# Optimization experiments

Hardware: AMD Instinct MI355X
Metric: run time of the kernel (lower is better)

## Reference

```python
import jax, jax.numpy as jnp
import numpy as np

B, N, D, R, E = 512, 32, 300, 5, 256
V_SENSE, V_GLOBAL = 20000, 50000  # last_idx_senses, last_idx_globals - last_idx_senses


def setup_inputs() -> dict:
    key = jax.random.key(0)
    ks = jax.random.split(key, 10)
    x = jax.random.normal(ks[0], (B, N, D), jnp.float32)
    edge_index = jax.random.randint(ks[1], (B, 2, E), 0, N)
    edge_type = jnp.sort(jax.random.randint(ks[2], (B, E), 0, R), axis=-1)
    # parameters (xavier-ish scales)
    conv_W = jax.random.normal(ks[3], (R, D, D), jnp.float32) * np.float32(1.0 / np.sqrt(D))
    W0 = jax.random.normal(ks[4], (D, D), jnp.float32) * np.float32(np.sqrt(2.0 / (D + D)))
    update_gate = jnp.ones((1,), jnp.float32)
    glob_W = jax.random.normal(ks[5], (V_GLOBAL, D), jnp.float32) * np.float32(1.0 / np.sqrt(D))
    glob_b = jnp.zeros((V_GLOBAL,), jnp.float32)
    sense_W = jax.random.normal(ks[6], (V_SENSE, D), jnp.float32) * np.float32(1.0 / np.sqrt(D))
    sense_b = jnp.zeros((V_SENSE,), jnp.float32)
    memory0 = jnp.zeros((N, D), jnp.float32)  # initial persisted memory (zeros vector broadcast)
    return dict(x=x, edge_index=edge_index, edge_type=edge_type, conv_W=conv_W, W0=W0,
                update_gate=update_gate, glob_W=glob_W, glob_b=glob_b,
                sense_W=sense_W, sense_b=sense_b, memory0=memory0)


def reference(x, edge_index, edge_type, conv_W, W0, update_gate, glob_W, glob_b, sense_W, sense_b, memory0):
    R_ = conv_W.shape[0]
    N_ = x.shape[1]

    def step(mem, inp):
        xs, ei, et = inp                      # [N,D], [2,E], [E]
        src, dst = ei[0], ei[1]
        # per-relation transformed features (GCNConv, bias=False)
        xw = jnp.einsum('nd,rde->rne', xs, conv_W)          # [R,N,D]
        # per-relation degrees with self-loops (PyG GCNConv symmetric norm)
        onehot = jax.nn.one_hot(et, R_, dtype=xs.dtype)     # [E,R]
        deg = 1.0 + jax.ops.segment_sum(onehot, dst, num_segments=N_)  # [N,R]
        dinv = jax.lax.rsqrt(deg)                           # [N,R]
        coeff = dinv[src, et] * dinv[dst, et]               # [E]
        msg = coeff[:, None] * xw[et, src]                  # [E,D]
        agg = jax.ops.segment_sum(msg, dst, num_segments=N_)  # sum over relations' convs
        self_term = jnp.einsum('rnd,nr->nd', xw, dinv * dinv)  # self-loop of each GCNConv
        composite = agg + self_term
        # prevlayer_connection = eye(N) @ (x @ W_0) = x @ W_0
        proposed = composite + xs @ W0
        new_mem = update_gate * proposed + (1.0 - update_gate) * mem  # rgcn_conv, persisted
        x1 = jax.nn.relu(new_mem)[0]                        # current node features [D]
        return new_mem, x1

    _, x1_all = jax.lax.scan(step, memory0, (x, edge_index, edge_type))  # [B,D]
    logits_g = x1_all @ glob_W.T + glob_b                   # [B,V_GLOBAL]
    logits_s = x1_all @ sense_W.T + sense_b                 # [B,V_SENSE]
    return (jax.nn.log_softmax(logits_g, axis=-1), jax.nn.log_softmax(logits_s, axis=-1))
```

## Files before the change

kernel.cpp:

```cpp
#include <hip/hip_runtime.h>
#include <stdint.h>

#define BDIM   512
#define NNODE  32
#define DDIM   300
#define NREL   5
#define NEDGE  256
#define VGLOB  50000
#define VSENSE 20000

#define K1PAD  1856
#define K2PAD  320
#define TG_GLOB  391
#define TG_SENSE 157
#define TGTOT  548
#define GROWS  50048
#define SROWS  20096
#define WROWS  70144
#define NCHUNK 3
#define KCH    10
#define NSCH   16
#define SCHL   32

typedef __attribute__((ext_vector_type(8))) short short8;
typedef __attribute__((ext_vector_type(4))) float f32x4;

__device__ __forceinline__ unsigned short f2bf(float x) {
    unsigned int u = __float_as_uint(x);
    u += 0x7fffu + ((u >> 16) & 1u);
    return (unsigned short)(u >> 16);
}

__device__ __forceinline__ float powi(float x, int n) {
    float r = 1.f, p = x;
    while (n) { if (n & 1) r *= p; p *= p; n >>= 1; }
    return r;
}

#define AS1 __attribute__((address_space(1)))
#define AS3 __attribute__((address_space(3)))
__device__ __forceinline__ void gload16(const void* gp, void* lp) {
    __builtin_amdgcn_global_load_lds((AS1 void*)gp, (AS3 void*)lp, 16, 0, 0);
}

__global__ __launch_bounds__(256) void k_prep_z(
    const float* __restrict__ x, const int* __restrict__ ei,
    const int* __restrict__ et, unsigned short* __restrict__ Zb)
{
    int b = blockIdx.x, t = threadIdx.x;
    __shared__ int   cnt[NNODE * NREL];
    __shared__ float dinv[NNODE * NREL];
    __shared__ int   ssrc[NEDGE];
    __shared__ int   sdst[NEDGE];
    __shared__ int   setp[NEDGE];
    __shared__ float z[6][DDIM];

    const int* src = ei + (size_t)b * 2 * NEDGE;
    const int* dst = src + NEDGE;
    const int* etb = et + (size_t)b * NEDGE;

    if (t < NNODE * NREL) cnt[t] = 0;
    __syncthreads();
    if (t < NEDGE) {
        int s = src[t], d = dst[t], r = etb[t];
        ssrc[t] = s; sdst[t] = d; setp[t] = r;
        atomicAdd(&cnt[d * NREL + r], 1);
    }
    __syncthreads();
    if (t < NNODE * NREL) dinv[t] = rsqrtf(1.0f + (float)cnt[t]);
    __syncthreads();

    const float* xb = x + (size_t)b * NNODE * DDIM;
    for (int d = t; d < DDIM; d += 256) {
        float x0 = xb[d];
#pragma unroll
        for (int r = 0; r < NREL; r++) { float c = dinv[r]; z[r][d] = c * c * x0; }
        z[5][d] = x0;
    }
    __syncthreads();
    for (int e = 0; e < NEDGE; e++) {
        if (sdst[e] != 0) continue;
        int s = ssrc[e], r = setp[e];
        float coeff = dinv[s * NREL + r] * dinv[r];
        const float* xs = xb + (size_t)s * DDIM;
        for (int d = t; d < DDIM; d += 256) z[r][d] += coeff * xs[d];
    }
    __syncthreads();
    unsigned short* zo = Zb + (size_t)b * K1PAD;
    for (int k = t; k < K1PAD; k += 256) {
        unsigned short v = 0;
        if (k < 6 * DDIM) { int r = k / DDIM, d = k - r * DDIM; v = f2bf(z[r][d]); }
        zo[k] = v;
    }
}

__global__ __launch_bounds__(256) void k_prep_w(
    const float* __restrict__ convW, const float* __restrict__ W0f,
    unsigned short* __restrict__ Wcb)
{
    int idx = blockIdx.x * 256 + threadIdx.x;
    if (idx >= 384 * K1PAD) return;
    int n = idx / K1PAD, k = idx - n * K1PAD;
    float v = 0.f;
    if (n < DDIM && k < 6 * DDIM) {
        int r = k / DDIM, d = k - r * DDIM;
        v = (r < NREL) ? convW[((size_t)r * DDIM + d) * DDIM + n]
                       : W0f[(size_t)d * DDIM + n];
    }
    Wcb[idx] = f2bf(v);
}

__global__ __launch_bounds__(256) void k_conv_w2(
    const float* __restrict__ globW, const float* __restrict__ senseW,
    unsigned short* __restrict__ Wgb)
{
    int idx = blockIdx.x * 256 + threadIdx.x;
    int row = idx / 80, kq = (idx - row * 80) * 4;
    unsigned int p0 = 0, p1 = 0;
    if (kq < DDIM) {
        const float* srcp = nullptr;
        if (row < GROWS) { if (row < VGLOB) srcp = globW + (size_t)row * DDIM; }
        else { int sr = row - GROWS; if (sr < VSENSE) srcp = senseW + (size_t)sr * DDIM; }
        if (srcp) {
            float4 v = *(const float4*)(srcp + kq);
            p0 = (unsigned int)f2bf(v.x) | ((unsigned int)f2bf(v.y) << 16);
            p1 = (unsigned int)f2bf(v.z) | ((unsigned int)f2bf(v.w) << 16);
        }
    }
    uint2 pp; pp.x = p0; pp.y = p1;
    *(uint2*)(Wgb + (size_t)row * K2PAD + kq) = pp;
}

template<int MODE>
__global__ __launch_bounds__(256) void k_gemm_b(
    const unsigned short* __restrict__ A, int ldk, int nk, int kchunk,
    int tiles0,
    const unsigned short* __restrict__ B0, int ldb0,
    const float* __restrict__ bias0, float* __restrict__ C0, long ldc0,
    int nstore0, const float* __restrict__ lse0, int tilebase0,
    const unsigned short* __restrict__ B1, int ldb1,
    const float* __restrict__ bias1, float* __restrict__ C1, long ldc1,
    int nstore1, const float* __restrict__ lse1, int tilebase1,
    float* __restrict__ pmax, float* __restrict__ psum)
{
    __shared__ __align__(16) char Alds[128 * 128];
    __shared__ __align__(16) char Blds[128 * 128];

    int t = threadIdx.x;
    int tile, mrep;
    if constexpr (MODE == 0) {
        tile = blockIdx.x; mrep = blockIdx.y;
    } else {
        int i = blockIdx.x + TGTOT * blockIdx.y;
        if (i < 2176) { int g = i >> 5, r = i & 31; tile = g * 8 + (r & 7); mrep = r >> 3; }
        else          { int j = i - 2176; tile = 544 + (j & 3); mrep = j >> 2; }
    }

    const unsigned short* Bp; const float *bias, *lse; float* Cout;
    long ldc; int ldb, nstore, tileidx, tloc;
    if (tile < tiles0) {
        Bp = B0; bias = bias0; Cout = C0; lse = lse0; ldc = ldc0;
        ldb = ldb0; nstore = nstore0; tloc = tile; tileidx = tilebase0 + tile;
    } else {
        tloc = tile - tiles0;
        Bp = B1; bias = bias1; Cout = C1; lse = lse1; ldc = ldc1;
        ldb = ldb1; nstore = nstore1; tileidx = tilebase1 + tloc;
    }
    int n0 = tloc * 128;
    int m0 = mrep * 128;

    int kt_lo = 0, kt_hi = nk >> 6;
    if constexpr (MODE == 0) {
        if (kchunk > 0) {
            kt_lo = blockIdx.z * kchunk;
            int hi = kt_lo + kchunk;
            if (hi < kt_hi) kt_hi = hi;
            Cout += (size_t)blockIdx.z * (BDIM * 304);
        }
    }

    int lane = t & 63, wid = t >> 6;
    int wm = wid >> 1, wn = wid & 1;
    int l15 = lane & 15, lq = lane >> 4;

    int trow = t >> 3;
    int sb = ((t & 7) << 4) ^ ((trow & 7) << 4);
    const char* Ag = (const char*)A + (size_t)(m0 + trow) * (ldk * 2) + sb;
    const char* Bg = (const char*)Bp + (size_t)(n0 + trow) * (ldb * 2) + sb;
    char* Al = Alds + t * 16;
    char* Bl = Blds + t * 16;
    size_t a32 = (size_t)32 * (ldk * 2);
    size_t b32 = (size_t)32 * (ldb * 2);

    int sw = (l15 & 7) << 4;
    int aoff0 = (lq * 16) ^ sw;
    int aoff1 = (64 + lq * 16) ^ sw;
    const char* Arow = Alds + (wm * 64 + l15) * 128;
    const char* Brow = Blds + (wn * 64 + l15) * 128;

    f32x4 acc[4][4] = {};

    for (int kt = kt_lo; kt < kt_hi; ++kt) {
        int k0b = kt << 7;
        const char* Agk = Ag + k0b;
        const char* Bgk = Bg + k0b;
#pragma unroll
        for (int c = 0; c < 4; c++) {
            gload16(Agk + c * a32, Al + c * 4096);
            gload16(Bgk + c * b32, Bl + c * 4096);
        }
        __syncthreads();
        short8 afr[4][2], bfr[4][2];
#pragma unroll
        for (int i = 0; i < 4; i++) {
            const char* Ab = Arow + i * (16 * 128);
            const char* Bb = Brow + i * (16 * 128);
            afr[i][0] = *(const short8*)(Ab + aoff0);
            afr[i][1] = *(const short8*)(Ab + aoff1);
            bfr[i][0] = *(const short8*)(Bb + aoff0);
            bfr[i][1] = *(const short8*)(Bb + aoff1);
        }
#pragma unroll
        for (int ks = 0; ks < 2; ks++)
#pragma unroll
            for (int mi = 0; mi < 4; mi++)
#pragma unroll
                for (int ni = 0; ni < 4; ni++)
                    acc[mi][ni] = __builtin_amdgcn_mfma_f32_16x16x32_bf16(
                        afr[mi][ks], bfr[ni][ks], acc[mi][ni], 0, 0, 0);
        __syncthreads();
    }

    if constexpr (MODE == 1) {
        __shared__ float sMax[128][2];
        __shared__ float sSum[128][2];
#pragma unroll
        for (int mi = 0; mi < 4; mi++) {
#pragma unroll
            for (int r = 0; r < 4; r++) {
                float vals[4];
                float rowmax = -3.0e38f;
#pragma unroll
                for (int ni = 0; ni < 4; ni++) {
                    int col = n0 + wn * 64 + ni * 16 + l15;
                    float v = -3.0e38f;
                    if (col < nstore) v = acc[mi][ni][r] + bias[col];
                    vals[ni] = v;
                    rowmax = fmaxf(rowmax, v);
                }
#pragma unroll
                for (int off = 1; off < 16; off <<= 1)
                    rowmax = fmaxf(rowmax, __shfl_xor(rowmax, off, 64));
                float s = 0.f;
#pragma unroll
                for (int ni = 0; ni < 4; ni++) s += __expf(vals[ni] - rowmax);
#pragma unroll
                for (int off = 1; off < 16; off <<= 1) s += __shfl_xor(s, off, 64);
                if (l15 == 0) {
                    int rl = wm * 64 + mi * 16 + lq * 4 + r;
                    sMax[rl][wn] = rowmax; sSum[rl][wn] = s;
                }
            }
        }
        __syncthreads();
        if (t < 128) {
            float ma = sMax[t][0], mb = sMax[t][1];
            float M = fmaxf(ma, mb);
            float S = sSum[t][0] * __expf(ma - M) + sSum[t][1] * __expf(mb - M);
            size_t o = (size_t)tileidx * BDIM + (m0 + t);
            pmax[o] = M; psum[o] = S;
        }
    } else {
#pragma unroll
        for (int mi = 0; mi < 4; mi++) {
            int row = m0 + wm * 64 + mi * 16 + lq * 4;
#pragma unroll
            for (int ni = 0; ni < 4; ni++) {
                int col = n0 + wn * 64 + ni * 16 + l15;
                if (col < nstore) {
#pragma unroll
                    for (int r = 0; r < 4; r++) {
                        float v = acc[mi][ni][r];
                        if constexpr (MODE == 2) v += bias[col] - lse[row + r];
                        Cout[(size_t)(row + r) * ldc + col] = v;
                    }
                }
            }
        }
    }
}

template<int MODE>
__global__ __launch_bounds__(256) void k_gemm_f32(
    const unsigned short* __restrict__ A, int ldk, int nk,
    int tiles0,
    const float* __restrict__ B0, int ldb0, int ksrc0, int brows0,
    const float* __restrict__ bias0, float* __restrict__ C0, long ldc0,
    int nstore0, const float* __restrict__ lse0, int tilebase0,
    const float* __restrict__ B1, int ldb1, int ksrc1, int brows1,
    const float* __restrict__ bias1, float* __restrict__ C1, long ldc1,
    int nstore1, const float* __restrict__ lse1, int tilebase1,
    float* __restrict__ pmax, float* __restrict__ psum)
{
    __shared__ __align__(16) short Alds[128 * 32];
    __shared__ __align__(16) short Blds[128 * 32];

    int t = threadIdx.x;
    int bx = blockIdx.x;
    const float* Bsrc; const float *bias, *lse; float* Cout;
    long ldc; int ldb, ksrc, brows, nstore, tileidx;
    if (bx < tiles0) {
        Bsrc = B0; bias = bias0; Cout = C0; lse = lse0; ldc = ldc0;
        ldb = ldb0; ksrc = ksrc0; brows = brows0; nstore = nstore0;
        tileidx = tilebase0 + bx;
    } else {
        bx -= tiles0;
        Bsrc = B1; bias = bias1; Cout = C1; lse = lse1; ldc = ldc1;
        ldb = ldb1; ksrc = ksrc1; brows = brows1; nstore = nstore1;
        tileidx = tilebase1 + bx;
    }
    int n0 = bx * 128;
    int m0 = blockIdx.y * 128;

    int lane = t & 63, wid = t >> 6;
    int wm = wid >> 1, wn = wid & 1;
    int l15 = lane & 15, lq = lane >> 4;

    f32x4 acc[4][4] = {};

    int arow = t >> 1, acol = (t & 1) * 16;
    const unsigned short* aptr = A + (size_t)(m0 + arow) * ldk + acol;
    int brow = t >> 3, bkq = (t & 7) * 4;

    int kt_hi = nk / 32;
    for (int kt = 0; kt < kt_hi; ++kt) {
        int k0 = kt * 32;
        uint4 a0 = *(const uint4*)(aptr + k0);
        uint4 a1 = *(const uint4*)(aptr + k0 + 8);
        float4 bv[4];
#pragma unroll
        for (int j = 0; j < 4; j++) {
            int row = n0 + brow + 32 * j;
            float4 v = {0.f, 0.f, 0.f, 0.f};
            if (row < brows && (k0 + bkq + 4) <= ksrc)
                v = *(const float4*)(Bsrc + (size_t)row * ldb + k0 + bkq);
            bv[j] = v;
        }
        __syncthreads();
        *(uint4*)&Alds[arow * 32 + acol] = a0;
        *(uint4*)&Alds[arow * 32 + acol + 8] = a1;
#pragma unroll
        for (int j = 0; j < 4; j++) {
            unsigned int p0 = (unsigned int)f2bf(bv[j].x) | ((unsigned int)f2bf(bv[j].y) << 16);
            unsigned int p1 = (unsigned int)f2bf(bv[j].z) | ((unsigned int)f2bf(bv[j].w) << 16);
            uint2 pp; pp.x = p0; pp.y = p1;
            *(uint2*)&Blds[(brow + 32 * j) * 32 + bkq] = pp;
        }
        __syncthreads();
        short8 afr[4], bfr[4];
#pragma unroll
        for (int i = 0; i < 4; i++) {
            afr[i] = *(const short8*)&Alds[(wm * 64 + i * 16 + l15) * 32 + lq * 8];
            bfr[i] = *(const short8*)&Blds[(wn * 64 + i * 16 + l15) * 32 + lq * 8];
        }
#pragma unroll
        for (int mi = 0; mi < 4; mi++)
#pragma unroll
            for (int ni = 0; ni < 4; ni++)
                acc[mi][ni] = __builtin_amdgcn_mfma_f32_16x16x32_bf16(
                    afr[mi], bfr[ni], acc[mi][ni], 0, 0, 0);
    }

    if constexpr (MODE == 1) {
        __shared__ float sMax[128][2];
        __shared__ float sSum[128][2];
#pragma unroll
        for (int mi = 0; mi < 4; mi++) {
#pragma unroll
            for (int r = 0; r < 4; r++) {
                float vals[4];
                float rowmax = -3.0e38f;
#pragma unroll
                for (int ni = 0; ni < 4; ni++) {
                    int col = n0 + wn * 64 + ni * 16 + l15;
                    float v = -3.0e38f;
                    if (col < nstore) v = acc[mi][ni][r] + bias[col];
                    vals[ni] = v;
                    rowmax = fmaxf(rowmax, v);
                }
#pragma unroll
                for (int off = 1; off < 16; off <<= 1)
                    rowmax = fmaxf(rowmax, __shfl_xor(rowmax, off, 64));
                float s = 0.f;
#pragma unroll
                for (int ni = 0; ni < 4; ni++) s += __expf(vals[ni] - rowmax);
#pragma unroll
                for (int off = 1; off < 16; off <<= 1) s += __shfl_xor(s, off, 64);
                if (l15 == 0) {
                    int rl = wm * 64 + mi * 16 + lq * 4 + r;
                    sMax[rl][wn] = rowmax; sSum[rl][wn] = s;
                }
            }
        }
        __syncthreads();
        if (t < 128) {
            float ma = sMax[t][0], mb = sMax[t][1];
            float M = fmaxf(ma, mb);
            float S = sSum[t][0] * __expf(ma - M) + sSum[t][1] * __expf(mb - M);
            size_t o = (size_t)tileidx * BDIM + (m0 + t);
            pmax[o] = M; psum[o] = S;
        }
    } else {
#pragma unroll
        for (int mi = 0; mi < 4; mi++) {
            int row = m0 + wm * 64 + mi * 16 + lq * 4;
#pragma unroll
            for (int ni = 0; ni < 4; ni++) {
                int col = n0 + wn * 64 + ni * 16 + l15;
                if (col < nstore) {
#pragma unroll
                    for (int r = 0; r < 4; r++) {
                        float v = acc[mi][ni][r];
                        if constexpr (MODE == 2) v += bias[col] - lse[row + r];
                        Cout[(size_t)(row + r) * ldc + col] = v;
                    }
                }
            }
        }
    }
}

__global__ __launch_bounds__(320) void k_scan_local(
    const float* __restrict__ prop, float* __restrict__ scanA,
    const float* __restrict__ gate)
{
    int d = threadIdx.x; if (d >= 304) return;
    int blk = blockIdx.x;
    float g = gate[0], og = 1.f - g;
    float m = 0.f;
    const float* p0 = prop + (size_t)blk * SCHL * 304 + d;
    const float* p1 = p0 + (size_t)BDIM * 304;
    const float* p2 = p1 + (size_t)BDIM * 304;
    float* o = scanA + (size_t)blk * SCHL * 304 + d;
#pragma unroll
    for (int i = 0; i < SCHL; i++) {
        size_t off = (size_t)i * 304;
        float pv = p0[off] + p1[off] + p2[off];
        m = g * pv + og * m;
        o[off] = m;
    }
}

__global__ __launch_bounds__(320) void k_scan_combine(
    const float* __restrict__ scanA, const float* __restrict__ gate,
    const float* __restrict__ mem0, float* __restrict__ mstart)
{
    int d = threadIdx.x; if (d >= DDIM) return;
    float g = gate[0], og = 1.f - g;
    float cS = powi(og, SCHL);
    float m = mem0[d];
#pragma unroll
    for (int blk = 0; blk < NSCH; blk++) {
        mstart[blk * 304 + d] = m;
        m = scanA[(size_t)(blk * SCHL + SCHL - 1) * 304 + d] + cS * m;
    }
}

__global__ __launch_bounds__(320) void k_finalize_x1(
    const float* __restrict__ scanA, const float* __restrict__ mstart,
    const float* __restrict__ gate, unsigned short* __restrict__ x1b)
{
    int b = blockIdx.x, d = threadIdx.x;
    unsigned short v = 0;
    if (d < DDIM) {
        float g = gate[0], og = 1.f - g;
        float mval = scanA[(size_t)b * 304 + d]
                   + powi(og, (b & (SCHL - 1)) + 1) * mstart[(b >> 5) * 304 + d];
        v = f2bf(fmaxf(mval, 0.f));
    }
    if (d < K2PAD) x1b[(size_t)b * K2PAD + d] = v;
}

__global__ __launch_bounds__(256) void k_lse_par(
    const float* __restrict__ pmax, const float* __restrict__ psum,
    float* __restrict__ lse)
{
    int b = blockIdx.x, seg = blockIdx.y, t = threadIdx.x;
    int base = seg ? TG_GLOB : 0;
    int nt = seg ? TG_SENSE : TG_GLOB;
    float M = -3.0e38f, S = 0.f;
    for (int i = t; i < nt; i += 256) {
        size_t o = (size_t)(base + i) * BDIM + b;
        float m = pmax[o], s = psum[o];
        if (m > M) { S = S * __expf(M - m) + s; M = m; }
        else       { S += s * __expf(m - M); }
    }
#pragma unroll
    for (int off = 1; off < 64; off <<= 1) {
        float Mo = __shfl_xor(M, off, 64), So = __shfl_xor(S, off, 64);
        float Mn = fmaxf(M, Mo);
        S = S * __expf(M - Mn) + So * __expf(Mo - Mn);
        M = Mn;
    }
    __shared__ float sM[4], sS[4];
    int lane = t & 63, wid = t >> 6;
    if (lane == 0) { sM[wid] = M; sS[wid] = S; }
    __syncthreads();
    if (t == 0) {
        M = sM[0]; S = sS[0];
#pragma unroll
        for (int w = 1; w < 4; w++) {
            float Mo = sM[w], So = sS[w];
            float Mn = fmaxf(M, Mo);
            S = S * __expf(M - Mn) + So * __expf(Mo - Mn);
            M = Mn;
        }
        lse[seg * BDIM + b] = M + __logf(S);
    }
}

extern "C" void kernel_launch(void* const* d_in, const int* in_sizes, int n_in,
                              void* d_out, int out_size, void* d_ws, size_t ws_size,
                              hipStream_t stream)
{
    (void)in_sizes; (void)n_in; (void)out_size;
    const float* x      = (const float*)d_in[0];
    const int*   ei     = (const int*)d_in[1];
    const int*   et     = (const int*)d_in[2];
    const float* convW  = (const float*)d_in[3];
    const float* W0f    = (const float*)d_in[4];
    const float* gate   = (const float*)d_in[5];
    const float* globW  = (const float*)d_in[6];
    const float* globB  = (const float*)d_in[7];
    const float* senseW = (const float*)d_in[8];
    const float* senseB = (const float*)d_in[9];
    const float* mem0   = (const float*)d_in[10];
    float* out = (float*)d_out;

    char* w = (char*)d_ws;
    unsigned short* Zb  = (unsigned short*)(w + 0);
    unsigned short* Wcb = (unsigned short*)(w + 1900544);
    unsigned short* x1b = (unsigned short*)(w + 3325952);
    float* prop         = (float*)(w + 3653632);
    float* scanA        = (float*)(w + 5521408);
    float* mstart       = (float*)(w + 6144000);
    float* pmax         = (float*)(w + 6163456);
    float* psum         = (float*)(w + 7285760);
    float* lse          = (float*)(w + 8408064);
    unsigned short* Wgb = (unsigned short*)(w + 8412160);
    const size_t WS_NEED_BIG = 8412160 + (size_t)WROWS * K2PAD * 2;
    bool bigws = ws_size >= WS_NEED_BIG;

    k_prep_z<<<BDIM, 256, 0, stream>>>(x, ei, et, Zb);
    k_prep_w<<<(384 * K1PAD + 255) / 256, 256, 0, stream>>>(convW, W0f, Wcb);
    if (bigws)
        k_conv_w2<<<(WROWS * 80) / 256, 256, 0, stream>>>(globW, senseW, Wgb);

    k_gemm_b<0><<<dim3(3, 4, NCHUNK), 256, 0, stream>>>(Zb, K1PAD, K1PAD, KCH,
        3, Wcb, K1PAD, nullptr, prop, 304, 304, nullptr, 0,
        nullptr, 0, nullptr, nullptr, 0, 0, nullptr, 0,
        nullptr, nullptr);

    k_scan_local<<<NSCH, 320, 0, stream>>>(prop, scanA, gate);
    k_scan_combine<<<1, 320, 0, stream>>>(scanA, gate, mem0, mstart);
    k_finalize_x1<<<BDIM, 320, 0, stream>>>(scanA, mstart, gate, x1b);

    if (bigws) {
        const unsigned short* WgbS = Wgb + (size_t)GROWS * K2PAD;
        k_gemm_b<1><<<dim3(TGTOT, 4), 256, 0, stream>>>(x1b, K2PAD, K2PAD, 0,
            TG_GLOB, Wgb, K2PAD, globB, nullptr, 0, VGLOB, nullptr, 0,
            WgbS, K2PAD, senseB, nullptr, 0, VSENSE, nullptr, TG_GLOB,
            pmax, psum);
        k_lse_par<<<dim3(BDIM, 2), 256, 0, stream>>>(pmax, psum, lse);
        k_gemm_b<2><<<dim3(TGTOT, 4), 256, 0, stream>>>(x1b, K2PAD, K2PAD, 0,
            TG_GLOB, Wgb, K2PAD, globB, out, VGLOB, VGLOB, lse, 0,
            WgbS, K2PAD, senseB, out + (size_t)BDIM * VGLOB, VSENSE, VSENSE, lse + BDIM, 0,
            nullptr, nullptr);
    } else {
        k_gemm_f32<1><<<dim3(TGTOT, 4), 256, 0, stream>>>(x1b, K2PAD, K2PAD,
            TG_GLOB, globW, DDIM, DDIM, VGLOB, globB, nullptr, 0, VGLOB, nullptr, 0,
            senseW, DDIM, DDIM, VSENSE, senseB, nullptr, 0, VSENSE, nullptr, TG_GLOB,
            pmax, psum);
        k_lse_par<<<dim3(BDIM, 2), 256, 0, stream>>>(pmax, psum, lse);
        k_gemm_f32<2><<<dim3(TGTOT, 4), 256, 0, stream>>>(x1b, K2PAD, K2PAD,
            TG_GLOB, globW, DDIM, DDIM, VGLOB, globB, out, VGLOB, VGLOB, lse, 0,
            senseW, DDIM, DDIM, VSENSE, senseB, out + (size_t)BDIM * VGLOB, VSENSE, VSENSE, lse + BDIM, 0,
            nullptr, nullptr);
    }
}
```

Before: 391.2 us.

## Write logits once in first GEMM pass and subtract LSE in a fixup pass

Replaces the two-pass log-softmax, which ran the vocabulary GEMM twice (once for partial max/sum, once to write outputs), with a single GEMM pass. That pass writes biased logits directly to the output along with the partial statistics, and a new fixup kernel then subtracts the row LSE in place. The three prep kernels are merged into one launch, and the scan-combine kernel is folded into finalize_x1. This removes a full GEMM recompute but adds an extra read-modify-write of the 140 MB output.

```diff
diff --git a/kernel.cpp b/kernel.cpp
--- a/kernel.cpp
+++ b/kernel.cpp
@@ -22,6 +22,10 @@
 #define NSCH   16
 #define SCHL   32
 
+#define NB_W2  21920
+#define NB_Z   512
+#define NB_W   2784
+
 typedef __attribute__((ext_vector_type(8))) short short8;
 typedef __attribute__((ext_vector_type(4))) float f32x4;
 
@@ -43,92 +47,96 @@
     __builtin_amdgcn_global_load_lds((AS1 void*)gp, (AS3 void*)lp, 16, 0, 0);
 }
 
-__global__ __launch_bounds__(256) void k_prep_z(
+__global__ __launch_bounds__(256) void k_prep_all(
     const float* __restrict__ x, const int* __restrict__ ei,
-    const int* __restrict__ et, unsigned short* __restrict__ Zb)
-{
-    int b = blockIdx.x, t = threadIdx.x;
-    __shared__ int   cnt[NNODE * NREL];
-    __shared__ float dinv[NNODE * NREL];
-    __shared__ int   ssrc[NEDGE];
-    __shared__ int   sdst[NEDGE];
-    __shared__ int   setp[NEDGE];
-    __shared__ float z[6][DDIM];
-
-    const int* src = ei + (size_t)b * 2 * NEDGE;
-    const int* dst = src + NEDGE;
-    const int* etb = et + (size_t)b * NEDGE;
-
-    if (t < NNODE * NREL) cnt[t] = 0;
-    __syncthreads();
-    if (t < NEDGE) {
-        int s = src[t], d = dst[t], r = etb[t];
-        ssrc[t] = s; sdst[t] = d; setp[t] = r;
-        atomicAdd(&cnt[d * NREL + r], 1);
-    }
-    __syncthreads();
-    if (t < NNODE * NREL) dinv[t] = rsqrtf(1.0f + (float)cnt[t]);
-    __syncthreads();
-
-    const float* xb = x + (size_t)b * NNODE * DDIM;
-    for (int d = t; d < DDIM; d += 256) {
-        float x0 = xb[d];
-#pragma unroll
-        for (int r = 0; r < NREL; r++) { float c = dinv[r]; z[r][d] = c * c * x0; }
-        z[5][d] = x0;
-    }
-    __syncthreads();
-    for (int e = 0; e < NEDGE; e++) {
-        if (sdst[e] != 0) continue;
-        int s = ssrc[e], r = setp[e];
-        float coeff = dinv[s * NREL + r] * dinv[r];
-        const float* xs = xb + (size_t)s * DDIM;
-        for (int d = t; d < DDIM; d += 256) z[r][d] += coeff * xs[d];
-    }
-    __syncthreads();
-    unsigned short* zo = Zb + (size_t)b * K1PAD;
-    for (int k = t; k < K1PAD; k += 256) {
-        unsigned short v = 0;
-        if (k < 6 * DDIM) { int r = k / DDIM, d = k - r * DDIM; v = f2bf(z[r][d]); }
-        zo[k] = v;
-    }
-}
-
-__global__ __launch_bounds__(256) void k_prep_w(
+    const int* __restrict__ et, unsigned short* __restrict__ Zb,
     const float* __restrict__ convW, const float* __restrict__ W0f,
-    unsigned short* __restrict__ Wcb)
-{
-    int idx = blockIdx.x * 256 + threadIdx.x;
-    if (idx >= 384 * K1PAD) return;
-    int n = idx / K1PAD, k = idx - n * K1PAD;
-    float v = 0.f;
-    if (n < DDIM && k < 6 * DDIM) {
-        int r = k / DDIM, d = k - r * DDIM;
-        v = (r < NREL) ? convW[((size_t)r * DDIM + d) * DDIM + n]
-                       : W0f[(size_t)d * DDIM + n];
-    }
-    Wcb[idx] = f2bf(v);
-}
-
-__global__ __launch_bounds__(256) void k_conv_w2(
+    unsigned short* __restrict__ Wcb,
     const float* __restrict__ globW, const float* __restrict__ senseW,
-    unsigned short* __restrict__ Wgb)
-{
-    int idx = blockIdx.x * 256 + threadIdx.x;
-    int row = idx / 80, kq = (idx - row * 80) * 4;
-    unsigned int p0 = 0, p1 = 0;
-    if (kq < DDIM) {
-        const float* srcp = nullptr;
-        if (row < GROWS) { if (row < VGLOB) srcp = globW + (size_t)row * DDIM; }
-        else { int sr = row - GROWS; if (sr < VSENSE) srcp = senseW + (size_t)sr * DDIM; }
-        if (srcp) {
-            float4 v = *(const float4*)(srcp + kq);
-            p0 = (unsigned int)f2bf(v.x) | ((unsigned int)f2bf(v.y) << 16);
-            p1 = (unsigned int)f2bf(v.z) | ((unsigned int)f2bf(v.w) << 16);
-        }
-    }
-    uint2 pp; pp.x = p0; pp.y = p1;
-    *(uint2*)(Wgb + (size_t)row * K2PAD + kq) = pp;
+    unsigned short* __restrict__ Wgb, int zbase)
+{
+    int blk = blockIdx.x, t = threadIdx.x;
+
+    if (blk < zbase) {
+        int idx = blk * 256 + t;
+        int row = idx / 80, kq = (idx - row * 80) * 4;
+        unsigned int p0 = 0, p1 = 0;
+        if (kq < DDIM) {
+            const float* srcp = nullptr;
+            if (row < GROWS) { if (row < VGLOB) srcp = globW + (size_t)row * DDIM; }
+            else { int sr = row - GROWS; if (sr < VSENSE) srcp = senseW + (size_t)sr * DDIM; }
+            if (srcp) {
+                float4 v = *(const float4*)(srcp + kq);
+                p0 = (unsigned int)f2bf(v.x) | ((unsigned int)f2bf(v.y) << 16);
+                p1 = (unsigned int)f2bf(v.z) | ((unsigned int)f2bf(v.w) << 16);
+            }
+        }
+        uint2 pp; pp.x = p0; pp.y = p1;
+        *(uint2*)(Wgb + (size_t)row * K2PAD + kq) = pp;
+        return;
+    }
+
+    if (blk < zbase + NB_Z) {
+        int b = blk - zbase;
+        __shared__ int   cnt[NNODE * NREL];
+        __shared__ float dinv[NNODE * NREL];
+        __shared__ int   ssrc[NEDGE];
+        __shared__ int   sdst[NEDGE];
+        __shared__ int   setp[NEDGE];
+        __shared__ float z[6][DDIM];
+
+        const int* src = ei + (size_t)b * 2 * NEDGE;
+        const int* dst = src + NEDGE;
+        const int* etb = et + (size_t)b * NEDGE;
+
+        if (t < NNODE * NREL) cnt[t] = 0;
+        __syncthreads();
+        if (t < NEDGE) {
+            int s = src[t], d = dst[t], r = etb[t];
+            ssrc[t] = s; sdst[t] = d; setp[t] = r;
+            atomicAdd(&cnt[d * NREL + r], 1);
+        }
+        __syncthreads();
+        if (t < NNODE * NREL) dinv[t] = rsqrtf(1.0f + (float)cnt[t]);
+        __syncthreads();
+
+        const float* xb = x + (size_t)b * NNODE * DDIM;
+        for (int d = t; d < DDIM; d += 256) {
+            float x0 = xb[d];
+#pragma unroll
+            for (int r = 0; r < NREL; r++) { float c = dinv[r]; z[r][d] = c * c * x0; }
+            z[5][d] = x0;
+        }
+        __syncthreads();
+        for (int e = 0; e < NEDGE; e++) {
+            if (sdst[e] != 0) continue;
+            int s = ssrc[e], r = setp[e];
+            float coeff = dinv[s * NREL + r] * dinv[r];
+            const float* xs = xb + (size_t)s * DDIM;
+            for (int d = t; d < DDIM; d += 256) z[r][d] += coeff * xs[d];
+        }
+        __syncthreads();
+        unsigned short* zo = Zb + (size_t)b * K1PAD;
+        for (int k = t; k < K1PAD; k += 256) {
+            unsigned short v = 0;
+            if (k < 6 * DDIM) { int r = k / DDIM, d = k - r * DDIM; v = f2bf(z[r][d]); }
+            zo[k] = v;
+        }
+        return;
+    }
+
+    {
+        int idx = (blk - zbase - NB_Z) * 256 + t;
+        if (idx >= 384 * K1PAD) return;
+        int n = idx / K1PAD, k = idx - n * K1PAD;
+        float v = 0.f;
+        if (n < DDIM && k < 6 * DDIM) {
+            int r = k / DDIM, d = k - r * DDIM;
+            v = (r < NREL) ? convW[((size_t)r * DDIM + d) * DDIM + n]
+                           : W0f[(size_t)d * DDIM + n];
+        }
+        Wcb[idx] = f2bf(v);
+    }
 }
 
 template<int MODE>
@@ -137,10 +145,10 @@
     int tiles0,
     const unsigned short* __restrict__ B0, int ldb0,
     const float* __restrict__ bias0, float* __restrict__ C0, long ldc0,
-    int nstore0, const float* __restrict__ lse0, int tilebase0,
+    int nstore0, int tilebase0,
     const unsigned short* __restrict__ B1, int ldb1,
     const float* __restrict__ bias1, float* __restrict__ C1, long ldc1,
-    int nstore1, const float* __restrict__ lse1, int tilebase1,
+    int nstore1, int tilebase1,
     float* __restrict__ pmax, float* __restrict__ psum)
 {
     __shared__ __align__(16) char Alds[128 * 128];
@@ -156,14 +164,14 @@
         else          { int j = i - 2176; tile = 544 + (j & 3); mrep = j >> 2; }
     }
 
-    const unsigned short* Bp; const float *bias, *lse; float* Cout;
+    const unsigned short* Bp; const float* bias; float* Cout;
     long ldc; int ldb, nstore, tileidx, tloc;
     if (tile < tiles0) {
-        Bp = B0; bias = bias0; Cout = C0; lse = lse0; ldc = ldc0;
+        Bp = B0; bias = bias0; Cout = C0; ldc = ldc0;
         ldb = ldb0; nstore = nstore0; tloc = tile; tileidx = tilebase0 + tile;
     } else {
         tloc = tile - tiles0;
-        Bp = B1; bias = bias1; Cout = C1; lse = lse1; ldc = ldc1;
+        Bp = B1; bias = bias1; Cout = C1; ldc = ldc1;
         ldb = ldb1; nstore = nstore1; tileidx = tilebase1 + tloc;
     }
     int n0 = tloc * 128;
@@ -236,6 +244,7 @@
         __shared__ float sSum[128][2];
 #pragma unroll
         for (int mi = 0; mi < 4; mi++) {
+            int row = m0 + wm * 64 + mi * 16 + lq * 4;
 #pragma unroll
             for (int r = 0; r < 4; r++) {
                 float vals[4];
@@ -249,6 +258,11 @@
                     rowmax = fmaxf(rowmax, v);
                 }
 #pragma unroll
+                for (int ni = 0; ni < 4; ni++) {
+                    int col = n0 + wn * 64 + ni * 16 + l15;
+                    if (col < nstore) Cout[(size_t)(row + r) * ldc + col] = vals[ni];
+                }
+#pragma unroll
                 for (int off = 1; off < 16; off <<= 1)
                     rowmax = fmaxf(rowmax, __shfl_xor(rowmax, off, 64));
                 float s = 0.f;
@@ -279,27 +293,23 @@
                 int col = n0 + wn * 64 + ni * 16 + l15;
                 if (col < nstore) {
 #pragma unroll
-                    for (int r = 0; r < 4; r++) {
-                        float v = acc[mi][ni][r];
-                        if constexpr (MODE == 2) v += bias[col] - lse[row + r];
-                        Cout[(size_t)(row + r) * ldc + col] = v;
-                    }
+                    for (int r = 0; r < 4; r++)
+                        Cout[(size_t)(row + r) * ldc + col] = acc[mi][ni][r];
                 }
             }
         }
     }
 }
 
-template<int MODE>
 __global__ __launch_bounds__(256) void k_gemm_f32(
     const unsigned short* __restrict__ A, int ldk, int nk,
     int tiles0,
     const float* __restrict__ B0, int ldb0, int ksrc0, int brows0,
     const float* __restrict__ bias0, float* __restrict__ C0, long ldc0,
-    int nstore0, const float* __restrict__ lse0, int tilebase0,
+    int nstore0, int tilebase0,
     const float* __restrict__ B1, int ldb1, int ksrc1, int brows1,
     const float* __restrict__ bias1, float* __restrict__ C1, long ldc1,
-    int nstore1, const float* __restrict__ lse1, int tilebase1,
+    int nstore1, int tilebase1,
     float* __restrict__ pmax, float* __restrict__ psum)
 {
     __shared__ __align__(16) short Alds[128 * 32];
@@ -307,15 +317,15 @@
 
     int t = threadIdx.x;
     int bx = blockIdx.x;
-    const float* Bsrc; const float *bias, *lse; float* Cout;
+    const float* Bsrc; const float* bias; float* Cout;
     long ldc; int ldb, ksrc, brows, nstore, tileidx;
     if (bx < tiles0) {
-        Bsrc = B0; bias = bias0; Cout = C0; lse = lse0; ldc = ldc0;
+        Bsrc = B0; bias = bias0; Cout = C0; ldc = ldc0;
         ldb = ldb0; ksrc = ksrc0; brows = brows0; nstore = nstore0;
         tileidx = tilebase0 + bx;
     } else {
         bx -= tiles0;
-        Bsrc = B1; bias = bias1; Cout = C1; lse = lse1; ldc = ldc1;
+        Bsrc = B1; bias = bias1; Cout = C1; ldc = ldc1;
         ldb = ldb1; ksrc = ksrc1; brows = brows1; nstore = nstore1;
         tileidx = tilebase1 + bx;
     }
@@ -371,62 +381,49 @@
                     afr[mi], bfr[ni], acc[mi][ni], 0, 0, 0);
     }
 
-    if constexpr (MODE == 1) {
-        __shared__ float sMax[128][2];
-        __shared__ float sSum[128][2];
-#pragma unroll
-        for (int mi = 0; mi < 4; mi++) {
-#pragma unroll
-            for (int r = 0; r < 4; r++) {
-                float vals[4];
-                float rowmax = -3.0e38f;
-#pragma unroll
-                for (int ni = 0; ni < 4; ni++) {
-                    int col = n0 + wn * 64 + ni * 16 + l15;
-                    float v = -3.0e38f;
-                    if (col < nstore) v = acc[mi][ni][r] + bias[col];
-                    vals[ni] = v;
-                    rowmax = fmaxf(rowmax, v);
-                }
-#pragma unroll
-                for (int off = 1; off < 16; off <<= 1)
-                    rowmax = fmaxf(rowmax, __shfl_xor(rowmax, off, 64));
-                float s = 0.f;
-#pragma unroll
-                for (int ni = 0; ni < 4; ni++) s += __expf(vals[ni] - rowmax);
-#pragma unroll
-                for (int off = 1; off < 16; off <<= 1) s += __shfl_xor(s, off, 64);
-                if (l15 == 0) {
-                    int rl = wm * 64 + mi * 16 + lq * 4 + r;
-                    sMax[rl][wn] = rowmax; sSum[rl][wn] = s;
-                }
-            }
-        }
-        __syncthreads();
-        if (t < 128) {
-            float ma = sMax[t][0], mb = sMax[t][1];
-            float M = fmaxf(ma, mb);
-            float S = sSum[t][0] * __expf(ma - M) + sSum[t][1] * __expf(mb - M);
-            size_t o = (size_t)tileidx * BDIM + (m0 + t);
-            pmax[o] = M; psum[o] = S;
-        }
-    } else {
-#pragma unroll
-        for (int mi = 0; mi < 4; mi++) {
-            int row = m0 + wm * 64 + mi * 16 + lq * 4;
+    __shared__ float sMax[128][2];
+    __shared__ float sSum[128][2];
+#pragma unroll
+    for (int mi = 0; mi < 4; mi++) {
+        int row = m0 + wm * 64 + mi * 16 + lq * 4;
+#pragma unroll
+        for (int r = 0; r < 4; r++) {
+            float vals[4];
+            float rowmax = -3.0e38f;
 #pragma unroll
             for (int ni = 0; ni < 4; ni++) {
                 int col = n0 + wn * 64 + ni * 16 + l15;
-                if (col < nstore) {
-#pragma unroll
-                    for (int r = 0; r < 4; r++) {
-                        float v = acc[mi][ni][r];
-                        if constexpr (MODE == 2) v += bias[col] - lse[row + r];
-                        Cout[(size_t)(row + r) * ldc + col] = v;
-                    }
-                }
+                float v = -3.0e38f;
+                if (col < nstore) v = acc[mi][ni][r] + bias[col];
+                vals[ni] = v;
+                rowmax = fmaxf(rowmax, v);
             }
-        }
+#pragma unroll
+            for (int ni = 0; ni < 4; ni++) {
+                int col = n0 + wn * 64 + ni * 16 + l15;
+                if (col < nstore) Cout[(size_t)(row + r) * ldc + col] = vals[ni];
+            }
+#pragma unroll
+            for (int off = 1; off < 16; off <<= 1)
+                rowmax = fmaxf(rowmax, __shfl_xor(rowmax, off, 64));
+            float s = 0.f;
+#pragma unroll
+            for (int ni = 0; ni < 4; ni++) s += __expf(vals[ni] - rowmax);
+#pragma unroll
+            for (int off = 1; off < 16; off <<= 1) s += __shfl_xor(s, off, 64);
+            if (l15 == 0) {
+                int rl = wm * 64 + mi * 16 + lq * 4 + r;
+                sMax[rl][wn] = rowmax; sSum[rl][wn] = s;
+            }
+        }
+    }
+    __syncthreads();
+    if (t < 128) {
+        float ma = sMax[t][0], mb = sMax[t][1];
+        float M = fmaxf(ma, mb);
+        float S = sSum[t][0] * __expf(ma - M) + sSum[t][1] * __expf(mb - M);
+        size_t o = (size_t)tileidx * BDIM + (m0 + t);
+        pmax[o] = M; psum[o] = S;
     }
 }
 
@@ -451,39 +448,29 @@
     }
 }
 
-__global__ __launch_bounds__(320) void k_scan_combine(
-    const float* __restrict__ scanA, const float* __restrict__ gate,
-    const float* __restrict__ mem0, float* __restrict__ mstart)
-{
-    int d = threadIdx.x; if (d >= DDIM) return;
-    float g = gate[0], og = 1.f - g;
-    float cS = powi(og, SCHL);
-    float m = mem0[d];
-#pragma unroll
-    for (int blk = 0; blk < NSCH; blk++) {
-        mstart[blk * 304 + d] = m;
-        m = scanA[(size_t)(blk * SCHL + SCHL - 1) * 304 + d] + cS * m;
-    }
-}
-
 __global__ __launch_bounds__(320) void k_finalize_x1(
-    const float* __restrict__ scanA, const float* __restrict__ mstart,
+    const float* __restrict__ scanA, const float* __restrict__ mem0,
     const float* __restrict__ gate, unsigned short* __restrict__ x1b)
 {
     int b = blockIdx.x, d = threadIdx.x;
     unsigned short v = 0;
     if (d < DDIM) {
         float g = gate[0], og = 1.f - g;
+        float cS = powi(og, SCHL);
+        int chunk = b >> 5;
+        float m = mem0[d];
+        for (int c = 0; c < chunk; c++)
+            m = scanA[(size_t)(c * SCHL + SCHL - 1) * 304 + d] + cS * m;
         float mval = scanA[(size_t)b * 304 + d]
-                   + powi(og, (b & (SCHL - 1)) + 1) * mstart[(b >> 5) * 304 + d];
+                   + powi(og, (b & (SCHL - 1)) + 1) * m;
         v = f2bf(fmaxf(mval, 0.f));
     }
     if (d < K2PAD) x1b[(size_t)b * K2PAD + d] = v;
 }
 
-__global__ __launch_bounds__(256) void k_lse_par(
+__global__ __launch_bounds__(256) void k_lse_fix(
     const float* __restrict__ pmax, const float* __restrict__ psum,
-    float* __restrict__ lse)
+    float* __restrict__ out)
 {
     int b = blockIdx.x, seg = blockIdx.y, t = threadIdx.x;
     int base = seg ? TG_GLOB : 0;
@@ -503,6 +490,7 @@
         M = Mn;
     }
     __shared__ float sM[4], sS[4];
+    __shared__ float sL;
     int lane = t & 63, wid = t >> 6;
     if (lane == 0) { sM[wid] = M; sS[wid] = S; }
     __syncthreads();
@@ -515,7 +503,18 @@
             S = S * __expf(M - Mn) + So * __expf(Mo - Mn);
             M = Mn;
         }
-        lse[seg * BDIM + b] = M + __logf(S);
+        sL = M + __logf(S);
+    }
+    __syncthreads();
+    float L = sL;
+    float* row = seg ? out + (size_t)BDIM * VGLOB + (size_t)b * VSENSE
+                     : out + (size_t)b * VGLOB;
+    int n4 = (seg ? VSENSE : VGLOB) >> 2;
+    float4* r4 = (float4*)row;
+    for (int i = t; i < n4; i += 256) {
+        float4 v = r4[i];
+        v.x -= L; v.y -= L; v.z -= L; v.w -= L;
+        r4[i] = v;
     }
 }
 
@@ -543,48 +542,36 @@
     unsigned short* x1b = (unsigned short*)(w + 3325952);
     float* prop         = (float*)(w + 3653632);
     float* scanA        = (float*)(w + 5521408);
-    float* mstart       = (float*)(w + 6144000);
-    float* pmax         = (float*)(w + 6163456);
-    float* psum         = (float*)(w + 7285760);
-    float* lse          = (float*)(w + 8408064);
-    unsigned short* Wgb = (unsigned short*)(w + 8412160);
-    const size_t WS_NEED_BIG = 8412160 + (size_t)WROWS * K2PAD * 2;
+    float* pmax         = (float*)(w + 6144000);
+    float* psum         = (float*)(w + 7266304);
+    unsigned short* Wgb = (unsigned short*)(w + 8388608);
+    const size_t WS_NEED_BIG = 8388608 + (size_t)WROWS * K2PAD * 2;
     bool bigws = ws_size >= WS_NEED_BIG;
 
-    k_prep_z<<<BDIM, 256, 0, stream>>>(x, ei, et, Zb);
-    k_prep_w<<<(384 * K1PAD + 255) / 256, 256, 0, stream>>>(convW, W0f, Wcb);
-    if (bigws)
-        k_conv_w2<<<(WROWS * 80) / 256, 256, 0, stream>>>(globW, senseW, Wgb);
+    int zbase = bigws ? NB_W2 : 0;
+    int nprep = zbase + NB_Z + NB_W;
+    k_prep_all<<<nprep, 256, 0, stream>>>(x, ei, et, Zb, convW, W0f, Wcb,
+                                          globW, senseW, Wgb, zbase);
 
     k_gemm_b<0><<<dim3(3, 4, NCHUNK), 256, 0, stream>>>(Zb, K1PAD, K1PAD, KCH,
-        3, Wcb, K1PAD, nullptr, prop, 304, 304, nullptr, 0,
-        nullptr, 0, nullptr, nullptr, 0, 0, nullptr, 0,
+        3, Wcb, K1PAD, nullptr, prop, 304, 304, 0,
+        nullptr, 0, nullptr, nullptr, 0, 0, 0,
         nullptr, nullptr);
 
     k_scan_local<<<NSCH, 320, 0, stream>>>(prop, scanA, gate);
-    k_scan_combine<<<1, 320, 0, stream>>>(scanA, gate, mem0, mstart);
-    k_finalize_x1<<<BDIM, 320, 0, stream>>>(scanA, mstart, gate, x1b);
+    k_finalize_x1<<<BDIM, 320, 0, stream>>>(scanA, mem0, gate, x1b);
 
     if (bigws) {
         const unsigned short* WgbS = Wgb + (size_t)GROWS * K2PAD;
         k_gemm_b<1><<<dim3(TGTOT, 4), 256, 0, stream>>>(x1b, K2PAD, K2PAD, 0,
-            TG_GLOB, Wgb, K2PAD, globB, nullptr, 0, VGLOB, nullptr, 0,
-            WgbS, K2PAD, senseB, nullptr, 0, VSENSE, nullptr, TG_GLOB,
+            TG_GLOB, Wgb, K2PAD, globB, out, VGLOB, VGLOB, 0,
+            WgbS, K2PAD, senseB, out + (size_t)BDIM * VGLOB, VSENSE, VSENSE, TG_GLOB,
             pmax, psum);
-        k_lse_par<<<dim3(BDIM, 2), 256, 0, stream>>>(pmax, psum, lse);
-        k_gemm_b<2><<<dim3(TGTOT, 4), 256, 0, stream>>>(x1b, K2PAD, K2PAD, 0,
-            TG_GLOB, Wgb, K2PAD, globB, out, VGLOB, VGLOB, lse, 0,
-            WgbS, K2PAD, senseB, out + (size_t)BDIM * VGLOB, VSENSE, VSENSE, lse + BDIM, 0,
-            nullptr, nullptr);
     } else {
-        k_gemm_f32<1><<<dim3(TGTOT, 4), 256, 0, stream>>>(x1b, K2PAD, K2PAD,
-            TG_GLOB, globW, DDIM, DDIM, VGLOB, globB, nullptr, 0, VGLOB, nullptr, 0,
-            senseW, DDIM, DDIM, VSENSE, senseB, nullptr, 0, VSENSE, nullptr, TG_GLOB,
+        k_gemm_f32<<<dim3(TGTOT, 4), 256, 0, stream>>>(x1b, K2PAD, K2PAD,
+            TG_GLOB, globW, DDIM, DDIM, VGLOB, globB, out, VGLOB, VGLOB, 0,
+            senseW, DDIM, DDIM, VSENSE, senseB, out + (size_t)BDIM * VGLOB, VSENSE, VSENSE, TG_GLOB,
             pmax, psum);
-        k_lse_par<<<dim3(BDIM, 2), 256, 0, stream>>>(pmax, psum, lse);
-        k_gemm_f32<2><<<dim3(TGTOT, 4), 256, 0, stream>>>(x1b, K2PAD, K2PAD,
-            TG_GLOB, globW, DDIM, DDIM, VGLOB, globB, out, VGLOB, VGLOB, lse, 0,
-            senseW, DDIM, DDIM, VSENSE, senseB, out + (size_t)BDIM * VGLOB, VSENSE, VSENSE, lse + BDIM, 0,
-            nullptr, nullptr);
-    }
-}
+    }
+    k_lse_fix<<<dim3(BDIM, 2), 256, 0, stream>>>(pmax, psum, out);
+}
```

Result: no change. 389.6 us (-0.4%).
